# Performance work log

Hardware: AMD Instinct MI355X
Metric: run time of the kernel (lower is better)

The kernel has to match this reference:

```python
import jax, jax.numpy as jnp
import numpy as np

N = 50000      # nodes
E = 800000     # edges (before self-loops)
DIN = 146      # input feature dim
D = 128        # hidden/out dim
G = 64         # graphs in batch
L = 4          # number of GCNConv layers (len(hidden_dims[1:]) + 1)
NC = 10        # classes
EPS = 1e-5     # BatchNorm eps


def setup_inputs() -> dict:
    key = jax.random.key(0)
    ks = jax.random.split(key, 12)
    x = jax.random.normal(ks[0], (N, DIN), jnp.float32)
    edge_index = jax.random.randint(ks[1], (2, E), 0, N, dtype=jnp.int64)
    batch = jnp.sort(jax.random.randint(ks[2], (N,), 0, G, dtype=jnp.int64))

    def lin(k, shape, fan_in):
        return (jax.random.normal(k, shape, jnp.float32) / np.sqrt(fan_in)).astype(jnp.float32)

    W_emb = lin(ks[3], (DIN, D), DIN)
    b_emb = jnp.zeros((D,), jnp.float32)
    W_gcn = lin(ks[4], (L, D, D), D)
    b_gcn = jnp.zeros((L, D), jnp.float32)
    bn_gamma = jnp.ones((L, D), jnp.float32)
    bn_beta = jnp.zeros((L, D), jnp.float32)
    W_r1 = lin(ks[5], (D, D // 2), D)
    b_r1 = jnp.zeros((D // 2,), jnp.float32)
    W_r2 = lin(ks[6], (D // 2, D // 4), D // 2)
    b_r2 = jnp.zeros((D // 4,), jnp.float32)
    W_r3 = lin(ks[7], (D // 4, NC), D // 4)
    b_r3 = jnp.zeros((NC,), jnp.float32)
    return {"x": x, "edge_index": edge_index, "batch": batch,
            "W_emb": W_emb, "b_emb": b_emb, "W_gcn": W_gcn, "b_gcn": b_gcn,
            "bn_gamma": bn_gamma, "bn_beta": bn_beta,
            "W_r1": W_r1, "b_r1": b_r1, "W_r2": W_r2, "b_r2": b_r2,
            "W_r3": W_r3, "b_r3": b_r3}


def reference(x, edge_index, batch, W_emb, b_emb, W_gcn, b_gcn,
              bn_gamma, bn_beta, W_r1, b_r1, W_r2, b_r2, W_r3, b_r3):
    # gcn_norm with self-loops (fill_value=1, improved=False)
    loop = jnp.arange(N, dtype=edge_index.dtype)
    src = jnp.concatenate([edge_index[0], loop])
    dst = jnp.concatenate([edge_index[1], loop])
    deg = jax.ops.segment_sum(jnp.ones(src.shape, x.dtype), dst, num_segments=N)
    dinv = jax.lax.rsqrt(jnp.maximum(deg, jnp.asarray(1e-12, x.dtype)))  # deg >= 1 (self loops)
    norm = (dinv[src] * dinv[dst])[:, None]  # [E+N, 1]

    h = x @ W_emb + b_emb  # embedding_h
    for l in range(L):
        h_in = h
        m = h @ W_gcn[l]                                            # [N, D]
        h = jax.ops.segment_sum(m[src] * norm, dst, num_segments=N) + b_gcn[l]
        # BatchNorm1d (training-mode batch stats, biased var)
        mu = h.mean(axis=0)
        var = h.var(axis=0)
        h = (h - mu) * jax.lax.rsqrt(var + EPS) * bn_gamma[l] + bn_beta[l]
        h = jax.nn.relu(h)
        h = h_in + h  # residual (dims always match here)

    # global_mean_pool over batch ids
    sums = jax.ops.segment_sum(h, batch, num_segments=G)
    cnts = jax.ops.segment_sum(jnp.ones((N, 1), h.dtype), batch, num_segments=G)
    hg = sums / jnp.maximum(cnts, 1.0)

    # MLPReadout: two hidden layers halving dims, then classifier
    z = jax.nn.relu(hg @ W_r1 + b_r1)
    z = jax.nn.relu(z @ W_r2 + b_r2)
    return z @ W_r3 + b_r3  # [G, NC]
```

## Files before the change

### kernel.cpp

```cpp
#include <hip/hip_runtime.h>
#include <hip/hip_bf16.h>

#define NN 50000
#define EE 800000
#define DIN 146
#define DD 128
#define GG 64
#define LL 4
#define NC 10
#define BN_EPS 1e-5f

#define KP_EMB 160
#define AST_L  136
#define NCOPY 64
#define NPW 4
#define RST 129

#define NBKT 196
#define BHP  200
#define NBE  782

#define A_EDGE   NBE
#define A_INIT   (A_EDGE + 256)
#define A_REPACK (A_INIT + 31250)
#define A_BATCH  (A_REPACK + 196)
#define A_PARAMS (A_BATCH + 384)
#define A_WT     (A_PARAMS + 400)

#define B_GEMM 391
#define C_TOT  (B_GEMM + NBE)

typedef __attribute__((ext_vector_type(8))) short bf16x8;
typedef __attribute__((ext_vector_type(4))) float f32x4;

__device__ __forceinline__ float bf2f(__hip_bfloat16 v) { return __bfloat162float(v); }
__device__ __forceinline__ float loadf(const void* p, long i, int f32) {
    return f32 ? ((const float*)p)[i] : bf2f(((const __hip_bfloat16*)p)[i]);
}
__device__ __forceinline__ unsigned short f2bf_bits(float f) {
    __hip_bfloat16 h = __float2bfloat16(f);
    return *(unsigned short*)&h;
}
__device__ __forceinline__ float bfu2f(unsigned short u) {
    return __uint_as_float((unsigned)u << 16);
}
__device__ __forceinline__ void acc_add8(float* acc, uint4 v) {
    acc[0] += __uint_as_float(v.x << 16);
    acc[1] += __uint_as_float(v.x & 0xffff0000u);
    acc[2] += __uint_as_float(v.y << 16);
    acc[3] += __uint_as_float(v.y & 0xffff0000u);
    acc[4] += __uint_as_float(v.z << 16);
    acc[5] += __uint_as_float(v.z & 0xffff0000u);
    acc[6] += __uint_as_float(v.w << 16);
    acc[7] += __uint_as_float(v.w & 0xffff0000u);
}
__device__ __forceinline__ ushort4 pack4(f32x4 v) {
    ushort4 u;
    u.x = f2bf_bits(v[0]); u.y = f2bf_bits(v[1]);
    u.z = f2bf_bits(v[2]); u.w = f2bf_bits(v[3]);
    return u;
}
__device__ __forceinline__ ushort4 pack4s(f32x4 v, float s) {
    ushort4 u;
    u.x = f2bf_bits(s * v[0]); u.y = f2bf_bits(s * v[1]);
    u.z = f2bf_bits(s * v[2]); u.w = f2bf_bits(s * v[3]);
    return u;
}

__device__ __forceinline__ int blk_excl_scan(int v, int t, int* wsum, int* total_sh) {
    __syncthreads();
    int lane = t & 63, w = t >> 6;
    int x = v;
    #pragma unroll
    for (int s = 1; s < 64; s <<= 1) {
        int y = __shfl_up(x, s, 64);
        if (lane >= s) x += y;
    }
    if (lane == 63) wsum[w] = x;
    __syncthreads();
    if (t == 0) {
        int a = 0;
        #pragma unroll
        for (int k = 0; k < 4; ++k) { int tmp = wsum[k]; wsum[k] = a; a += tmp; }
        *total_sh = a;
    }
    __syncthreads();
    return x - v + wsum[w];
}

__global__ void detect_kernel(const void* ei, const void* batch, const void* Wemb,
                              int* __restrict__ flags) {
    __shared__ int s_edge_nz, s_batch_nz, s_f32_cnt;
    int t = threadIdx.x;
    if (t == 0) { s_edge_nz = 0; s_batch_nz = 0; s_f32_cnt = 0; }
    __syncthreads();
    {   const int* w = (const int*)ei;
        long j = ((long)t * ((2L * EE) / 64)) | 1;
        if (w[j] != 0) atomicAdd(&s_edge_nz, 1);
    }
    {   const int* w = (const int*)batch;
        long j = ((long)(NN / 2) + (long)t * ((NN / 2) / 64)) | 1;
        if (j < NN && w[j] != 0) atomicAdd(&s_batch_nz, 1);
    }
    {   const unsigned short* w = (const unsigned short*)Wemb;
        unsigned short v = w[2 * t];
        int ex = (v >> 7) & 0xFF;
        if (v != 0 && ex >= 128) atomicAdd(&s_f32_cnt, 1);
    }
    __syncthreads();
    if (t == 0) {
        flags[0] = (s_edge_nz == 0) ? 1 : 0;
        flags[1] = (s_batch_nz == 0) ? 1 : 0;
        flags[2] = (s_f32_cnt >= 8) ? 1 : 0;
    }
}

struct Param { const void* src; float* dst; int src_n; int dst_n; };
struct Params12 { Param p[12]; };
struct WtDesc { const void* src; long src_off; unsigned short* dst; int K; int Kpad; };
struct WtDescs5 { WtDesc p[5]; };

__global__ __launch_bounds__(256) void mega_conv_kernel(
    const void* __restrict__ x, const void* __restrict__ ei,
    const void* __restrict__ batch, const int* __restrict__ flags,
    unsigned short* __restrict__ xb, float* __restrict__ statmulti,
    float* __restrict__ hgsum, int* __restrict__ b32,
    unsigned* __restrict__ pk, unsigned char* __restrict__ bkt,
    int* __restrict__ bh, Params12 P, WtDescs5 W)
{
    int b = blockIdx.x;
    int t = threadIdx.x;
    if (b < A_EDGE) {
        __shared__ int hist[NBKT];
        if (t < NBKT) hist[t] = 0;
        __syncthreads();
        int e0 = (b * 256 + t) * 4;
        if (e0 < EE) {
            const int* w = (const int*)ei;
            int4 sv, dv;
            if (flags[0]) {
                int4 u0 = *(const int4*)(w + 2L * e0);
                int4 u1 = *(const int4*)(w + 2L * e0 + 4);
                int4 v0 = *(const int4*)(w + 2L * (EE + e0));
                int4 v1 = *(const int4*)(w + 2L * (EE + e0) + 4);
                sv = make_int4(u0.x, u0.z, u1.x, u1.z);
                dv = make_int4(v0.x, v0.z, v1.x, v1.z);
            } else {
                sv = *(const int4*)(w + e0);
                dv = *(const int4*)(w + EE + e0);
            }
            int ss[4] = {sv.x, sv.y, sv.z, sv.w};
            int dd2[4] = {dv.x, dv.y, dv.z, dv.w};
            unsigned pk4[4], bk4[4];
            #pragma unroll
            for (int k = 0; k < 4; ++k) {
                unsigned s = min((unsigned)ss[k], (unsigned)(NN - 1));
                unsigned d = min((unsigned)dd2[k], (unsigned)(NN - 1));
                pk4[k] = (s << 8) | (d & 255u);
                bk4[k] = d >> 8;
                atomicAdd(&hist[bk4[k]], 1);
            }
            *(uint4*)(pk + e0) = make_uint4(pk4[0], pk4[1], pk4[2], pk4[3]);
            *(uchar4*)(bkt + e0) = make_uchar4((unsigned char)bk4[0], (unsigned char)bk4[1],
                                               (unsigned char)bk4[2], (unsigned char)bk4[3]);
        }
        __syncthreads();
        if (t < NBKT) bh[b * BHP + t] = hist[t];
    } else if (b < A_INIT) {
        int i = (b - A_EDGE) * 256 + t;
        if (i < LL * NCOPY * 256) statmulti[i] = 0.0f;
        if (i < GG * DD) hgsum[i] = 0.0f;
    } else if (b < A_REPACK) {
        int f32 = flags[2];
        long idx = (long)(b - A_INIT) * 256 + t;
        int row = (int)(idx / KP_EMB);
        int k = (int)(idx - (long)row * KP_EMB);
        float v = (k < DIN) ? loadf(x, (long)row * DIN + k, f32) : 0.0f;
        xb[idx] = f2bf_bits(v);
    } else if (b < A_BATCH) {
        int i = (b - A_REPACK) * 256 + t;
        if (i < NN) b32[i] = flags[1] ? ((const int*)batch)[2L * i] : ((const int*)batch)[i];
    } else if (b < A_PARAMS) {
        int f32 = flags[2];
        int bb = b - A_BATCH;
        const Param& e = P.p[bb >> 5];
        int idx = (bb & 31) * 256 + t;
        if (idx < e.dst_n)
            e.dst[idx] = (idx < e.src_n) ? loadf(e.src, idx, f32) : 0.0f;
    } else {
        int f32 = flags[2];
        int bb = b - A_PARAMS;
        int y = bb / 80;
        const WtDesc& e = W.p[y];
        int idx = (bb - y * 80) * 256 + t;
        if (idx < 128 * e.Kpad) {
            int n = idx / e.Kpad, k = idx - n * e.Kpad;
            float v = (k < e.K) ? loadf(e.src, e.src_off + (long)k * DD + n, f32) : 0.0f;
            e.dst[idx] = f2bf_bits(v);
        }
    }
}

__global__ __launch_bounds__(256) void bscan_kernel(int* __restrict__ bh, int* __restrict__ tot) {
    __shared__ int wsum[4], total_sh;
    int b = blockIdx.x;
    int t = threadIdx.x;
    int carry = 0;
    #pragma unroll 1
    for (int c = 0; c < 4; ++c) {
        int i = c * 256 + t;
        int v = (i < NBE) ? bh[i * BHP + b] : 0;
        int excl = blk_excl_scan(v, t, wsum, &total_sh);
        if (i < NBE) bh[i * BHP + b] = excl + carry;
        carry += total_sh;
    }
    if (t == 0) tot[b] = carry;
}

__global__ void bscan2_kernel(const int* __restrict__ tot, int* __restrict__ base,
                              int* __restrict__ off_last) {
    __shared__ int wsum[4], total_sh;
    int t = threadIdx.x;
    int v = (t < NBKT) ? tot[t] : 0;
    int excl = blk_excl_scan(v, t, wsum, &total_sh);
    if (t < NBKT) base[t] = excl;
    if (t == 0) { base[NBKT] = total_sh; *off_last = total_sh; }
}


__global__ __launch_bounds__(256) void bucket_emb_kernel(
    const unsigned* __restrict__ pk, const unsigned char* __restrict__ bkt,
    const int* __restrict__ bh, const int* __restrict__ base,
    unsigned* __restrict__ bucketA,
    const unsigned short* __restrict__ Ab,
    const unsigned short* __restrict__ Wt,
    const float* __restrict__ bias,
    unsigned short* __restrict__ hb, int n)
{
    int t = threadIdx.x;
    if (blockIdx.x >= B_GEMM) {
        int bb = blockIdx.x - B_GEMM;
        __shared__ int cur[NBKT];
        if (t < NBKT) cur[t] = bh[bb * BHP + t] + base[t];
        __syncthreads();
        int e0 = (bb * 256 + t) * 4;
        if (e0 < EE) {
            uint4 p4 = *(const uint4*)(pk + e0);
            uchar4 b4 = *(const uchar4*)(bkt + e0);
            unsigned pks[4] = {p4.x, p4.y, p4.z, p4.w};
            unsigned bks[4] = {b4.x, b4.y, b4.z, b4.w};
            #pragma unroll
            for (int k = 0; k < 4; ++k) {
                int slot = atomicAdd(&cur[bks[k]], 1);
                bucketA[slot] = pks[k];
            }
        }
        return;
    }
    int r0 = blockIdx.x * 128;
    int lane = t & 63, w = t >> 6;
    int m = lane & 15, quad = lane >> 4;
    int rbase = r0 + w * 32;
    bf16x8 a[2][5];
    #pragma unroll
    for (int rt = 0; rt < 2; ++rt)
        #pragma unroll
        for (int c = 0; c < 5; ++c) {
            int rr = rbase + rt * 16 + m; if (rr > n - 1) rr = n - 1;
            a[rt][c] = *(const bf16x8*)(Ab + (long)rr * KP_EMB + c * 32 + quad * 8);
        }
    f32x4 acc[2][8];
    #pragma unroll
    for (int t8 = 0; t8 < 8; ++t8) {
        float4 bv = *(const float4*)&bias[t8 * 16 + quad * 4];
        f32x4 ai = {bv.x, bv.y, bv.z, bv.w};
        acc[0][t8] = ai; acc[1][t8] = ai;
    }
    #pragma unroll
    for (int t8 = 0; t8 < 8; ++t8) {
        #pragma unroll
        for (int c = 0; c < 5; ++c) {
            bf16x8 b = *(const bf16x8*)(Wt + (long)(t8 * 16 + m) * KP_EMB + c * 32 + quad * 8);
            acc[0][t8] = __builtin_amdgcn_mfma_f32_16x16x32_bf16(b, a[0][c], acc[0][t8], 0, 0, 0);
            acc[1][t8] = __builtin_amdgcn_mfma_f32_16x16x32_bf16(b, a[1][c], acc[1][t8], 0, 0, 0);
        }
    }
    #pragma unroll
    for (int rt = 0; rt < 2; ++rt) {
        int row = rbase + rt * 16 + m;
        if (row < n) {
            #pragma unroll
            for (int t8 = 0; t8 < 8; ++t8)
                *(ushort4*)(hb + (long)row * DD + t8 * 16 + quad * 4) = pack4(acc[rt][t8]);
        }
    }
}

__global__ __launch_bounds__(256) void csr_kernel(
    const unsigned* __restrict__ bucketA, const int* __restrict__ base,
    int* __restrict__ off, float* __restrict__ dinv, int* __restrict__ src_s)
{
    __shared__ int dg[256], cur[256], wsum[4], total_sh;
    int b = blockIdx.x, t = threadIdx.x;
    int eb0 = base[b], eb1 = base[b + 1];
    dg[t] = 0;
    __syncthreads();
    for (int e = eb0 + t; e < eb1; e += 256)
        atomicAdd(&dg[bucketA[e] & 255u], 1);
    __syncthreads();
    int v = dg[t];
    int excl = blk_excl_scan(v, t, wsum, &total_sh);
    int node = b * 256 + t;
    if (node < NN) {
        off[node] = eb0 + excl;
        dinv[node] = rsqrtf((float)(v + 1));
    }
    cur[t] = excl;
    __syncthreads();
    for (int e = eb0 + t; e < eb1; e += 256) {
        unsigned pv = bucketA[e];
        int r = atomicAdd(&cur[pv & 255u], 1);
        src_s[eb0 + r] = (int)(pv >> 8);
    }
}

__global__ __launch_bounds__(256) void gemm_plain_kernel(
    const unsigned short* __restrict__ Ab,
    const unsigned short* __restrict__ Wt,
    const float* __restrict__ dinv,
    unsigned short* __restrict__ Mb, int n)
{
    int t = threadIdx.x;
    int r0 = blockIdx.x * 128;
    int lane = t & 63, w = t >> 6;
    int m = lane & 15, quad = lane >> 4;
    int rbase = r0 + w * 32;
    bf16x8 a[2][4];
    #pragma unroll
    for (int rt = 0; rt < 2; ++rt)
        #pragma unroll
        for (int c = 0; c < 4; ++c) {
            int rr = rbase + rt * 16 + m; if (rr > n - 1) rr = n - 1;
            a[rt][c] = *(const bf16x8*)(Ab + (long)rr * DD + c * 32 + quad * 8);
        }
    float dvt[2];
    int rowt[2];
    #pragma unroll
    for (int rt = 0; rt < 2; ++rt) {
        int rr = rbase + rt * 16 + m;
        rowt[rt] = rr;
        if (rr > n - 1) rr = n - 1;
        dvt[rt] = dinv[rr];
    }
    f32x4 acc[2][8];
    #pragma unroll
    for (int t8 = 0; t8 < 8; ++t8) {
        f32x4 z = {0.f, 0.f, 0.f, 0.f};
        acc[0][t8] = z; acc[1][t8] = z;
    }
    #pragma unroll
    for (int t8 = 0; t8 < 8; ++t8) {
        #pragma unroll
        for (int c = 0; c < 4; ++c) {
            bf16x8 b = *(const bf16x8*)(Wt + (long)(t8 * 16 + m) * DD + c * 32 + quad * 8);
            acc[0][t8] = __builtin_amdgcn_mfma_f32_16x16x32_bf16(b, a[0][c], acc[0][t8], 0, 0, 0);
            acc[1][t8] = __builtin_amdgcn_mfma_f32_16x16x32_bf16(b, a[1][c], acc[1][t8], 0, 0, 0);
        }
    }
    #pragma unroll
    for (int rt = 0; rt < 2; ++rt) {
        if (rowt[rt] < n) {
            #pragma unroll
            for (int t8 = 0; t8 < 8; ++t8)
                *(ushort4*)(Mb + (long)rowt[rt] * DD + t8 * 16 + quad * 4) = pack4s(acc[rt][t8], dvt[rt]);
        }
    }
}

__global__ __launch_bounds__(256) void gemm_fused_kernel(
    const unsigned short* __restrict__ aggb, unsigned short* __restrict__ hb,
    const float* __restrict__ statmulti, const float* __restrict__ gamma,
    const float* __restrict__ beta, const float* __restrict__ dinv,
    const unsigned short* __restrict__ Wt, unsigned short* __restrict__ Mb, int n)
{
    __shared__ unsigned short As[128 * AST_L];
    __shared__ float bnsh[256];
    int t = threadIdx.x;
    int r0 = blockIdx.x * 128;
    {
        float s = 0.0f;
        #pragma unroll 8
        for (int k = 0; k < NCOPY; ++k) s += statmulti[k * 256 + t];
        bnsh[t] = s;
    }
    __syncthreads();
    {
        int c4 = (t & 31) * 4, rsub = t >> 5;
        float inv_n = 1.0f / (float)n;
        float4 sm = *(const float4*)&bnsh[c4];
        float4 sq = *(const float4*)&bnsh[128 + c4];
        float4 ga = *(const float4*)&gamma[c4];
        float4 be = *(const float4*)&beta[c4];
        float4 mu, rs;
        mu.x = sm.x * inv_n; mu.y = sm.y * inv_n; mu.z = sm.z * inv_n; mu.w = sm.w * inv_n;
        rs.x = rsqrtf(sq.x * inv_n - mu.x * mu.x + BN_EPS) * ga.x;
        rs.y = rsqrtf(sq.y * inv_n - mu.y * mu.y + BN_EPS) * ga.y;
        rs.z = rsqrtf(sq.z * inv_n - mu.z * mu.z + BN_EPS) * ga.z;
        rs.w = rsqrtf(sq.w * inv_n - mu.w * mu.w + BN_EPS) * ga.w;
        #pragma unroll 4
        for (int i = 0; i < 16; ++i) {
            int row = i * 8 + rsub;
            int r = r0 + row;
            unsigned short o0 = 0, o1 = 0, o2 = 0, o3 = 0;
            if (r < n) {
                long g = (long)r * DD + c4;
                ushort4 au = *(const ushort4*)&aggb[g];
                ushort4 hu = *(const ushort4*)&hb[g];
                float h0 = bfu2f(hu.x) + fmaxf((bfu2f(au.x) - mu.x) * rs.x + be.x, 0.0f);
                float h1 = bfu2f(hu.y) + fmaxf((bfu2f(au.y) - mu.y) * rs.y + be.y, 0.0f);
                float h2 = bfu2f(hu.z) + fmaxf((bfu2f(au.z) - mu.z) * rs.z + be.z, 0.0f);
                float h3 = bfu2f(hu.w) + fmaxf((bfu2f(au.w) - mu.w) * rs.w + be.w, 0.0f);
                o0 = f2bf_bits(h0); o1 = f2bf_bits(h1);
                o2 = f2bf_bits(h2); o3 = f2bf_bits(h3);
                ushort4 ho; ho.x = o0; ho.y = o1; ho.z = o2; ho.w = o3;
                *(ushort4*)&hb[g] = ho;
            }
            unsigned short* dst = &As[row * AST_L + c4];
            dst[0] = o0; dst[1] = o1; dst[2] = o2; dst[3] = o3;
        }
    }
    __syncthreads();
    int lane = t & 63, w = t >> 6;
    int m = lane & 15, quad = lane >> 4;
    int rl = w * 32;
    int rbase = r0 + rl;
    bf16x8 a[2][4];
    #pragma unroll
    for (int rt = 0; rt < 2; ++rt)
        #pragma unroll
        for (int c = 0; c < 4; ++c)
            a[rt][c] = *(const bf16x8*)(As + (rl + rt * 16 + m) * AST_L + c * 32 + quad * 8);
    float dvt[2];
    int rowt[2];
    #pragma unroll
    for (int rt = 0; rt < 2; ++rt) {
        int rr = rbase + rt * 16 + m;
        rowt[rt] = rr;
        if (rr > n - 1) rr = n - 1;
        dvt[rt] = dinv[rr];
    }
    f32x4 acc[2][8];
    #pragma unroll
    for (int t8 = 0; t8 < 8; ++t8) {
        f32x4 z = {0.f, 0.f, 0.f, 0.f};
        acc[0][t8] = z; acc[1][t8] = z;
    }
    #pragma unroll
    for (int t8 = 0; t8 < 8; ++t8) {
        #pragma unroll
        for (int c = 0; c < 4; ++c) {
            bf16x8 b = *(const bf16x8*)(Wt + (long)(t8 * 16 + m) * DD + c * 32 + quad * 8);
            acc[0][t8] = __builtin_amdgcn_mfma_f32_16x16x32_bf16(b, a[0][c], acc[0][t8], 0, 0, 0);
            acc[1][t8] = __builtin_amdgcn_mfma_f32_16x16x32_bf16(b, a[1][c], acc[1][t8], 0, 0, 0);
        }
    }
    #pragma unroll
    for (int rt = 0; rt < 2; ++rt) {
        if (rowt[rt] < n) {
            #pragma unroll
            for (int t8 = 0; t8 < 8; ++t8)
                *(ushort4*)(Mb + (long)rowt[rt] * DD + t8 * 16 + quad * 4) = pack4s(acc[rt][t8], dvt[rt]);
        }
    }
}

__global__ __launch_bounds__(256) void agg_kernel(
    const unsigned short* __restrict__ mb, const int* __restrict__ off,
    const int* __restrict__ src_s,
    const float* __restrict__ dinv, const float* __restrict__ bias,
    unsigned short* __restrict__ aggb, float* __restrict__ statacc)
{
    __shared__ float sred[4][4 * RST];
    __shared__ float2 ssum[4][64], ssq[4][64];
    int t = threadIdx.x;
    int wv = t >> 6, lane = t & 63;
    int grp = lane >> 4, sl = lane & 15;
    float* red = sred[wv];
    float2 bi = ((const float2*)bias)[lane];
    float2 sAcc = {0.0f, 0.0f}, qAcc = {0.0f, 0.0f};
    int i0 = (blockIdx.x * 4 + wv) * NPW;
    #pragma unroll 1
    for (int ni = 0; ni < NPW; ++ni) {
        int i = i0 + ni;
        if (i >= NN) break;
        float acc[8];
        #pragma unroll
        for (int k = 0; k < 8; ++k) acc[k] = 0.0f;
        if (grp == 0) {
            uint4 v = *(const uint4*)(mb + (long)i * DD + sl * 8);
            acc_add8(acc, v);
        }
        int e  = off[i];
        int e1 = off[i + 1];
        for (; e + 16 <= e1; e += 16) {
            int j0 = src_s[e + grp];
            int j1 = src_s[e + 4 + grp];
            int j2 = src_s[e + 8 + grp];
            int j3 = src_s[e + 12 + grp];
            uint4 v0 = *(const uint4*)(mb + (long)j0 * DD + sl * 8);
            uint4 v1 = *(const uint4*)(mb + (long)j1 * DD + sl * 8);
            uint4 v2 = *(const uint4*)(mb + (long)j2 * DD + sl * 8);
            uint4 v3 = *(const uint4*)(mb + (long)j3 * DD + sl * 8);
            acc_add8(acc, v0);
            acc_add8(acc, v1);
            acc_add8(acc, v2);
            acc_add8(acc, v3);
        }
        for (; e + 8 <= e1; e += 8) {
            int ja = src_s[e + grp];
            int jb = src_s[e + 4 + grp];
            uint4 va = *(const uint4*)(mb + (long)ja * DD + sl * 8);
            uint4 vb = *(const uint4*)(mb + (long)jb * DD + sl * 8);
            acc_add8(acc, va);
            acc_add8(acc, vb);
        }
        for (; e + 4 <= e1; e += 4) {
            int j = src_s[e + grp];
            uint4 v = *(const uint4*)(mb + (long)j * DD + sl * 8);
            acc_add8(acc, v);
        }
        if (e + grp < e1) {
            int j = src_s[e + grp];
            uint4 v = *(const uint4*)(mb + (long)j * DD + sl * 8);
            acc_add8(acc, v);
        }
        #pragma unroll
        for (int k = 0; k < 8; ++k) red[grp * RST + sl * 8 + k] = acc[k];
        asm volatile("" ::: "memory");
        float c0 = 0.0f, c1 = 0.0f;
        #pragma unroll
        for (int g = 0; g < 4; ++g) {
            c0 += red[g * RST + 2 * lane];
            c1 += red[g * RST + 2 * lane + 1];
        }
        asm volatile("" ::: "memory");
        float di = dinv[i];
        float o0 = di * c0 + bi.x;
        float o1 = di * c1 + bi.y;
        unsigned packed = ((unsigned)f2bf_bits(o1) << 16) | f2bf_bits(o0);
        ((unsigned*)aggb)[(long)i * 64 + lane] = packed;
        sAcc.x += o0; sAcc.y += o1;
        qAcc.x += o0 * o0; qAcc.y += o1 * o1;
    }
    ssum[wv][lane] = sAcc; ssq[wv][lane] = qAcc;
    __syncthreads();
    if (wv == 0) {
        float2 s0 = ssum[0][lane], s1 = ssum[1][lane], s2 = ssum[2][lane], s3 = ssum[3][lane];
        float2 q0 = ssq[0][lane], q1 = ssq[1][lane], q2 = ssq[2][lane], q3 = ssq[3][lane];
        float sx = s0.x + s1.x + s2.x + s3.x;
        float sy = s0.y + s1.y + s2.y + s3.y;
        float qx = q0.x + q1.x + q2.x + q3.x;
        float qy = q0.y + q1.y + q2.y + q3.y;
        float* copy = statacc + (blockIdx.x & (NCOPY - 1)) * 256;
        atomicAdd(&copy[2 * lane], sx);
        atomicAdd(&copy[2 * lane + 1], sy);
        atomicAdd(&copy[128 + 2 * lane], qx);
        atomicAdd(&copy[128 + 2 * lane + 1], qy);
    }
}

__global__ void pool1_kernel(const unsigned short* __restrict__ hb,
                             const unsigned short* __restrict__ aggb,
                             const float* __restrict__ statmulti,
                             const float* __restrict__ gamma, const float* __restrict__ beta,
                             const int* __restrict__ b32, float* __restrict__ hgsum, int n) {
    __shared__ float bnsh[256];
    int t = threadIdx.x;
    {
        float s = 0.0f;
        #pragma unroll 8
        for (int k = 0; k < NCOPY; ++k) s += statmulti[k * 256 + t];
        bnsh[t] = s;
    }
    __syncthreads();
    int c4 = (t & 31) * 4, rsub = t >> 5;
    float inv_n = 1.0f / (float)n;
    float4 sm = *(const float4*)&bnsh[c4];
    float4 sq = *(const float4*)&bnsh[128 + c4];
    float4 ga = *(const float4*)&gamma[c4];
    float4 be = *(const float4*)&beta[c4];
    float4 mu, rs;
    mu.x = sm.x * inv_n; mu.y = sm.y * inv_n; mu.z = sm.z * inv_n; mu.w = sm.w * inv_n;
    rs.x = rsqrtf(sq.x * inv_n - mu.x * mu.x + BN_EPS) * ga.x;
    rs.y = rsqrtf(sq.y * inv_n - mu.y * mu.y + BN_EPS) * ga.y;
    rs.z = rsqrtf(sq.z * inv_n - mu.z * mu.z + BN_EPS) * ga.z;
    rs.w = rsqrtf(sq.w * inv_n - mu.w * mu.w + BN_EPS) * ga.w;
    int rows_pb = (n + gridDim.x - 1) / gridDim.x;
    int r0 = blockIdx.x * rows_pb;
    int r1 = min(n, r0 + rows_pb);
    float4 acc = {0, 0, 0, 0};
    int gcur = -1;
    for (int r = r0 + rsub; r < r1; r += 8) {
        int g = b32[r];
        if (g != gcur) {
            if (gcur >= 0) {
                atomicAdd(&hgsum[gcur * DD + c4 + 0], acc.x);
                atomicAdd(&hgsum[gcur * DD + c4 + 1], acc.y);
                atomicAdd(&hgsum[gcur * DD + c4 + 2], acc.z);
                atomicAdd(&hgsum[gcur * DD + c4 + 3], acc.w);
            }
            acc.x = acc.y = acc.z = acc.w = 0.0f;
            gcur = ((unsigned)g < (unsigned)GG) ? g : -1;
        }
        if (gcur >= 0) {
            long ix = (long)r * DD + c4;
            ushort4 au = *(const ushort4*)&aggb[ix];
            ushort4 hu = *(const ushort4*)&hb[ix];
            acc.x += bfu2f(hu.x) + fmaxf((bfu2f(au.x) - mu.x) * rs.x + be.x, 0.0f);
            acc.y += bfu2f(hu.y) + fmaxf((bfu2f(au.y) - mu.y) * rs.y + be.y, 0.0f);
            acc.z += bfu2f(hu.z) + fmaxf((bfu2f(au.z) - mu.z) * rs.z + be.z, 0.0f);
            acc.w += bfu2f(hu.w) + fmaxf((bfu2f(au.w) - mu.w) * rs.w + be.w, 0.0f);
        }
    }
    if (gcur >= 0) {
        atomicAdd(&hgsum[gcur * DD + c4 + 0], acc.x);
        atomicAdd(&hgsum[gcur * DD + c4 + 1], acc.y);
        atomicAdd(&hgsum[gcur * DD + c4 + 2], acc.z);
        atomicAdd(&hgsum[gcur * DD + c4 + 3], acc.w);
    }
}

__device__ int lower_bound_i(const int* __restrict__ a, int n, int v) {
    int lo = 0, hi = n;
    while (lo < hi) {
        int mid = (lo + hi) >> 1;
        if (a[mid] < v) lo = mid + 1; else hi = mid;
    }
    return lo;
}

__global__ void readout_kernel(const float* __restrict__ hgsum, const int* __restrict__ b32,
                               const float* __restrict__ W1, const float* __restrict__ b1,
                               const float* __restrict__ W2, const float* __restrict__ b2,
                               const float* __restrict__ W3, const float* __restrict__ b3,
                               const int* __restrict__ flags, void* __restrict__ out, int n) {
    int f32 = flags[2];
    int g = blockIdx.x;
    int t = threadIdx.x;
    __shared__ float hgs[DD];
    __shared__ float z1[DD / 2];
    __shared__ float z2[DD / 4];
    int lo = lower_bound_i(b32, n, g);
    int hi = lower_bound_i(b32, n, g + 1);
    float invc = 1.0f / fmaxf((float)(hi - lo), 1.0f);
    hgs[t] = hgsum[g * DD + t] * invc;
    __syncthreads();
    if (t < DD / 2) {
        float acc = b1[t];
        #pragma unroll 8
        for (int k = 0; k < DD; ++k) acc = fmaf(hgs[k], W1[k * (DD / 2) + t], acc);
        z1[t] = fmaxf(acc, 0.0f);
    }
    __syncthreads();
    if (t < DD / 4) {
        float acc = b2[t];
        #pragma unroll 8
        for (int k = 0; k < DD / 2; ++k) acc = fmaf(z1[k], W2[k * (DD / 4) + t], acc);
        z2[t] = fmaxf(acc, 0.0f);
    }
    __syncthreads();
    if (t < NC) {
        float acc = b3[t];
        #pragma unroll 8
        for (int k = 0; k < DD / 4; ++k) acc = fmaf(z2[k], W3[k * NC + t], acc);
        if (f32) ((float*)out)[g * NC + t] = acc;
        else     ((__hip_bfloat16*)out)[g * NC + t] = __float2bfloat16(acc);
    }
}

extern "C" void kernel_launch(void* const* d_in, const int* in_sizes, int n_in,
                              void* d_out, int out_size, void* d_ws, size_t ws_size,
                              hipStream_t stream) {
    const void* x      = d_in[0];
    const void* ei     = d_in[1];
    const void* batch  = d_in[2];
    const void* W_emb  = d_in[3];
    const void* b_emb  = d_in[4];
    const void* W_gcn  = d_in[5];
    const void* b_gcn  = d_in[6];
    const void* bn_g   = d_in[7];
    const void* bn_b   = d_in[8];
    const void* W_r1   = d_in[9];
    const void* b_r1   = d_in[10];
    const void* W_r2   = d_in[11];
    const void* b_r2   = d_in[12];
    const void* W_r3   = d_in[13];
    const void* b_r3   = d_in[14];

    char* p = (char*)d_ws;
    auto alloc = [&](size_t bytes) -> void* {
        void* r = (void*)p;
        p += (bytes + 255) & ~(size_t)255;
        return r;
    };
    int*   flags  = (int*)alloc(64 * 4);
    float* statmulti = (float*)alloc((size_t)LL * NCOPY * 256 * 4);
    float* hgsum  = (float*)alloc((size_t)GG * DD * 4);
    int*   off    = (int*)alloc((size_t)(NN + 1) * 4);
    float* dinv   = (float*)alloc((size_t)NN * 4);
    int*   b32    = (int*)alloc((size_t)NN * 4);
    int*   src_s  = (int*)alloc((size_t)EE * 4);
    unsigned* pk  = (unsigned*)alloc((size_t)EE * 4);
    unsigned char* bkt = (unsigned char*)alloc((size_t)EE);
    int*   bh     = (int*)alloc((size_t)NBE * BHP * 4);
    int*   tot    = (int*)alloc(256 * 4);
    int*   base   = (int*)alloc(256 * 4);
    unsigned* bucketA = (unsigned*)alloc((size_t)EE * 4);
    unsigned short* hb = (unsigned short*)alloc((size_t)NN * DD * 2);
    unsigned short* mb = (unsigned short*)alloc((size_t)NN * DD * 2);
    unsigned short* aggb = (unsigned short*)alloc((size_t)NN * DD * 2);
    unsigned short* xb = (unsigned short*)alloc((size_t)NN * KP_EMB * 2);
    unsigned short* wt_emb = (unsigned short*)alloc((size_t)DD * KP_EMB * 2);
    unsigned short* wt_gcn = (unsigned short*)alloc((size_t)LL * DD * DD * 2);
    float* b_emb32 = (float*)alloc(DD * 4);
    float* b_gcn32 = (float*)alloc((size_t)LL * DD * 4);
    float* bng32   = (float*)alloc((size_t)LL * DD * 4);
    float* bnb32   = (float*)alloc((size_t)LL * DD * 4);
    float* wr1     = (float*)alloc((size_t)DD * (DD / 2) * 4);
    float* br1     = (float*)alloc((DD / 2) * 4);
    float* wr2     = (float*)alloc((size_t)(DD / 2) * (DD / 4) * 4);
    float* br2     = (float*)alloc((DD / 4) * 4);
    float* wr3     = (float*)alloc((size_t)(DD / 4) * NC * 4);
    float* br3     = (float*)alloc(NC * 4);

    detect_kernel<<<1, 64, 0, stream>>>(ei, batch, W_emb, flags);

    Params12 P;
    P.p[0]  = { b_emb, b_emb32, DD, DD };
    P.p[1]  = { b_gcn, b_gcn32, LL * DD, LL * DD };
    P.p[2]  = { bn_g,  bng32,   LL * DD, LL * DD };
    P.p[3]  = { bn_b,  bnb32,   LL * DD, LL * DD };
    P.p[4]  = { W_r1,  wr1,     DD * (DD / 2), DD * (DD / 2) };
    P.p[5]  = { b_r1,  br1,     DD / 2, DD / 2 };
    P.p[6]  = { W_r2,  wr2,     (DD / 2) * (DD / 4), (DD / 2) * (DD / 4) };
    P.p[7]  = { b_r2,  br2,     DD / 4, DD / 4 };
    P.p[8]  = { W_r3,  wr3,     (DD / 4) * NC, (DD / 4) * NC };
    P.p[9]  = { b_r3,  br3,     NC, NC };
    P.p[10] = { b_r3,  br3,     0, 0 };
    P.p[11] = { b_r3,  br3,     0, 0 };

    WtDescs5 W;
    W.p[0] = { W_emb, 0,            wt_emb,                DIN, KP_EMB };
    W.p[1] = { W_gcn, 0L * DD * DD, wt_gcn + 0L * DD * DD, DD,  DD };
    W.p[2] = { W_gcn, 1L * DD * DD, wt_gcn + 1L * DD * DD, DD,  DD };
    W.p[3] = { W_gcn, 2L * DD * DD, wt_gcn + 2L * DD * DD, DD,  DD };
    W.p[4] = { W_gcn, 3L * DD * DD, wt_gcn + 3L * DD * DD, DD,  DD };

    mega_conv_kernel<<<A_WT, 256, 0, stream>>>(x, ei, batch, flags, xb, statmulti,
                                               hgsum, b32, pk, bkt, bh, P, W);

    bscan_kernel<<<NBKT, 256, 0, stream>>>(bh, tot);
    bscan2_kernel<<<1, 256, 0, stream>>>(tot, base, off + NN);

    bucket_emb_kernel<<<C_TOT, 256, 0, stream>>>(pk, bkt, bh, base, bucketA,
                                                 xb, wt_emb, b_emb32, hb, NN);

    csr_kernel<<<NBKT, 256, 0, stream>>>(bucketA, base, off, dinv, src_s);

    gemm_plain_kernel<<<(NN + 127) / 128, 256, 0, stream>>>(hb, wt_gcn, dinv, mb, NN);

    int ngemm = (NN + 127) / 128;
    int nagg = (NN + 4 * NPW - 1) / (4 * NPW);
    for (int l = 0; l < LL; ++l) {
        if (l > 0) {
            gemm_fused_kernel<<<ngemm, 256, 0, stream>>>(
                aggb, hb, statmulti + (size_t)(l - 1) * NCOPY * 256,
                bng32 + (l - 1) * DD, bnb32 + (l - 1) * DD,
                dinv, wt_gcn + (size_t)l * DD * DD, mb, NN);
        }
        agg_kernel<<<nagg, 256, 0, stream>>>(mb, off, src_s, dinv,
                                             b_gcn32 + l * DD, aggb,
                                             statmulti + (size_t)l * NCOPY * 256);
    }

    pool1_kernel<<<512, 256, 0, stream>>>(hb, aggb, statmulti + (size_t)(LL - 1) * NCOPY * 256,
                                          bng32 + (LL - 1) * DD, bnb32 + (LL - 1) * DD,
                                          b32, hgsum, NN);
    readout_kernel<<<GG, DD, 0, stream>>>(hgsum, b32, wr1, br1, wr2, br2, wr3, br3,
                                          flags, d_out, NN);
}
```

Measured before the change: 413.3 us.

## Aggregate full rows per wave lane-wise and vectorize input repacking

```diff
diff --git a/kernel.cpp b/kernel.cpp
--- a/kernel.cpp
+++ b/kernel.cpp
@@ -14,7 +14,6 @@
 #define AST_L  136
 #define NCOPY 64
 #define NPW 4
-#define RST 129
 
 #define NBKT 196
 #define BHP  200
@@ -22,7 +21,7 @@
 
 #define A_EDGE   NBE
 #define A_INIT   (A_EDGE + 256)
-#define A_REPACK (A_INIT + 31250)
+#define A_REPACK (A_INIT + 3907)
 #define A_BATCH  (A_REPACK + 196)
 #define A_PARAMS (A_BATCH + 384)
 #define A_WT     (A_PARAMS + 400)
@@ -44,16 +43,8 @@
 __device__ __forceinline__ float bfu2f(unsigned short u) {
     return __uint_as_float((unsigned)u << 16);
 }
-__device__ __forceinline__ void acc_add8(float* acc, uint4 v) {
-    acc[0] += __uint_as_float(v.x << 16);
-    acc[1] += __uint_as_float(v.x & 0xffff0000u);
-    acc[2] += __uint_as_float(v.y << 16);
-    acc[3] += __uint_as_float(v.y & 0xffff0000u);
-    acc[4] += __uint_as_float(v.z << 16);
-    acc[5] += __uint_as_float(v.z & 0xffff0000u);
-    acc[6] += __uint_as_float(v.w << 16);
-    acc[7] += __uint_as_float(v.w & 0xffff0000u);
-}
+__device__ __forceinline__ float lo16(unsigned v) { return __uint_as_float(v << 16); }
+__device__ __forceinline__ float hi16(unsigned v) { return __uint_as_float(v & 0xffff0000u); }
 __device__ __forceinline__ ushort4 pack4(f32x4 v) {
     ushort4 u;
     u.x = f2bf_bits(v[0]); u.y = f2bf_bits(v[1]);
@@ -172,11 +163,43 @@
         if (i < GG * DD) hgsum[i] = 0.0f;
     } else if (b < A_REPACK) {
         int f32 = flags[2];
-        long idx = (long)(b - A_INIT) * 256 + t;
-        int row = (int)(idx / KP_EMB);
-        int k = (int)(idx - (long)row * KP_EMB);
-        float v = (k < DIN) ? loadf(x, (long)row * DIN + k, f32) : 0.0f;
-        xb[idx] = f2bf_bits(v);
+        long idx8 = (long)(b - A_INIT) * 256 + t;
+        if (idx8 < (long)NN * 20) {
+            int row = (int)(idx8 / 20);
+            int c8 = (int)(idx8 - (long)row * 20) * 8;
+            float v[8];
+            if (c8 + 8 <= DIN) {
+                if (f32) {
+                    const float* xp = (const float*)x + (long)row * DIN + c8;
+                    #pragma unroll
+                    for (int k2 = 0; k2 < 4; ++k2) {
+                        float2 f = *(const float2*)(xp + 2 * k2);
+                        v[2 * k2] = f.x; v[2 * k2 + 1] = f.y;
+                    }
+                } else {
+                    const unsigned* xp = (const unsigned*)((const unsigned short*)x +
+                                                           (long)row * DIN + c8);
+                    #pragma unroll
+                    for (int k2 = 0; k2 < 4; ++k2) {
+                        unsigned u = xp[k2];
+                        v[2 * k2] = bfu2f((unsigned short)u);
+                        v[2 * k2 + 1] = bfu2f((unsigned short)(u >> 16));
+                    }
+                }
+            } else {
+                #pragma unroll
+                for (int k = 0; k < 8; ++k) {
+                    int col = c8 + k;
+                    v[k] = (col < DIN) ? loadf(x, (long)row * DIN + col, f32) : 0.0f;
+                }
+            }
+            unsigned o[4];
+            #pragma unroll
+            for (int k2 = 0; k2 < 4; ++k2)
+                o[k2] = (unsigned)f2bf_bits(v[2 * k2]) |
+                        ((unsigned)f2bf_bits(v[2 * k2 + 1]) << 16);
+            *(uint4*)(xb + (long)row * KP_EMB + c8) = make_uint4(o[0], o[1], o[2], o[3]);
+        }
     } else if (b < A_BATCH) {
         int i = (b - A_REPACK) * 256 + t;
         if (i < NN) b32[i] = flags[1] ? ((const int*)batch)[2L * i] : ((const int*)batch)[i];
@@ -475,17 +498,14 @@
 }
 
 __global__ __launch_bounds__(256) void agg_kernel(
-    const unsigned short* __restrict__ mb, const int* __restrict__ off,
+    const unsigned* __restrict__ mb32, const int* __restrict__ off,
     const int* __restrict__ src_s,
     const float* __restrict__ dinv, const float* __restrict__ bias,
-    unsigned short* __restrict__ aggb, float* __restrict__ statacc)
+    unsigned* __restrict__ aggb32, float* __restrict__ statacc)
 {
-    __shared__ float sred[4][4 * RST];
     __shared__ float2 ssum[4][64], ssq[4][64];
     int t = threadIdx.x;
     int wv = t >> 6, lane = t & 63;
-    int grp = lane >> 4, sl = lane & 15;
-    float* red = sred[wv];
     float2 bi = ((const float2*)bias)[lane];
     float2 sAcc = {0.0f, 0.0f}, qAcc = {0.0f, 0.0f};
     int i0 = (blockIdx.x * 4 + wv) * NPW;
@@ -493,62 +513,49 @@
     for (int ni = 0; ni < NPW; ++ni) {
         int i = i0 + ni;
         if (i >= NN) break;
-        float acc[8];
-        #pragma unroll
-        for (int k = 0; k < 8; ++k) acc[k] = 0.0f;
-        if (grp == 0) {
-            uint4 v = *(const uint4*)(mb + (long)i * DD + sl * 8);
-            acc_add8(acc, v);
-        }
-        int e  = off[i];
-        int e1 = off[i + 1];
-        for (; e + 16 <= e1; e += 16) {
-            int j0 = src_s[e + grp];
-            int j1 = src_s[e + 4 + grp];
-            int j2 = src_s[e + 8 + grp];
-            int j3 = src_s[e + 12 + grp];
-            uint4 v0 = *(const uint4*)(mb + (long)j0 * DD + sl * 8);
-            uint4 v1 = *(const uint4*)(mb + (long)j1 * DD + sl * 8);
-            uint4 v2 = *(const uint4*)(mb + (long)j2 * DD + sl * 8);
-            uint4 v3 = *(const uint4*)(mb + (long)j3 * DD + sl * 8);
-            acc_add8(acc, v0);
-            acc_add8(acc, v1);
-            acc_add8(acc, v2);
-            acc_add8(acc, v3);
-        }
+        int e = off[i], e1 = off[i + 1];
+        unsigned vs = mb32[(long)i * 64 + lane];
+        float a0 = lo16(vs), a1 = hi16(vs);
         for (; e + 8 <= e1; e += 8) {
-            int ja = src_s[e + grp];
-            int jb = src_s[e + 4 + grp];
-            uint4 va = *(const uint4*)(mb + (long)ja * DD + sl * 8);
-            uint4 vb = *(const uint4*)(mb + (long)jb * DD + sl * 8);
-            acc_add8(acc, va);
-            acc_add8(acc, vb);
+            int j0 = src_s[e + 0], j1 = src_s[e + 1], j2 = src_s[e + 2], j3 = src_s[e + 3];
+            int j4 = src_s[e + 4], j5 = src_s[e + 5], j6 = src_s[e + 6], j7 = src_s[e + 7];
+            unsigned v0 = mb32[(long)j0 * 64 + lane];
+            unsigned v1 = mb32[(long)j1 * 64 + lane];
+            unsigned v2 = mb32[(long)j2 * 64 + lane];
+            unsigned v3 = mb32[(long)j3 * 64 + lane];
+            unsigned v4 = mb32[(long)j4 * 64 + lane];
+            unsigned v5 = mb32[(long)j5 * 64 + lane];
+            unsigned v6 = mb32[(long)j6 * 64 + lane];
+            unsigned v7 = mb32[(long)j7 * 64 + lane];
+            a0 += lo16(v0); a1 += hi16(v0);
+            a0 += lo16(v1); a1 += hi16(v1);
+            a0 += lo16(v2); a1 += hi16(v2);
+            a0 += lo16(v3); a1 += hi16(v3);
+            a0 += lo16(v4); a1 += hi16(v4);
+            a0 += lo16(v5); a1 += hi16(v5);
+            a0 += lo16(v6); a1 += hi16(v6);
+            a0 += lo16(v7); a1 += hi16(v7);
         }
         for (; e + 4 <= e1; e += 4) {
-            int j = src_s[e + grp];
-            uint4 v = *(const uint4*)(mb + (long)j * DD + sl * 8);
-            acc_add8(acc, v);
-        }
-        if (e + grp < e1) {
-            int j = src_s[e + grp];
-            uint4 v = *(const uint4*)(mb + (long)j * DD + sl * 8);
-            acc_add8(acc, v);
-        }
-        #pragma unroll
-        for (int k = 0; k < 8; ++k) red[grp * RST + sl * 8 + k] = acc[k];
-        asm volatile("" ::: "memory");
-        float c0 = 0.0f, c1 = 0.0f;
-        #pragma unroll
-        for (int g = 0; g < 4; ++g) {
-            c0 += red[g * RST + 2 * lane];
-            c1 += red[g * RST + 2 * lane + 1];
-        }
-        asm volatile("" ::: "memory");
+            int j0 = src_s[e + 0], j1 = src_s[e + 1], j2 = src_s[e + 2], j3 = src_s[e + 3];
+            unsigned v0 = mb32[(long)j0 * 64 + lane];
+            unsigned v1 = mb32[(long)j1 * 64 + lane];
+            unsigned v2 = mb32[(long)j2 * 64 + lane];
+            unsigned v3 = mb32[(long)j3 * 64 + lane];
+            a0 += lo16(v0); a1 += hi16(v0);
+            a0 += lo16(v1); a1 += hi16(v1);
+            a0 += lo16(v2); a1 += hi16(v2);
+            a0 += lo16(v3); a1 += hi16(v3);
+        }
+        for (; e < e1; ++e) {
+            int j = src_s[e];
+            unsigned v = mb32[(long)j * 64 + lane];
+            a0 += lo16(v); a1 += hi16(v);
+        }
         float di = dinv[i];
-        float o0 = di * c0 + bi.x;
-        float o1 = di * c1 + bi.y;
-        unsigned packed = ((unsigned)f2bf_bits(o1) << 16) | f2bf_bits(o0);
-        ((unsigned*)aggb)[(long)i * 64 + lane] = packed;
+        float o0 = fmaf(di, a0, bi.x);
+        float o1 = fmaf(di, a1, bi.y);
+        aggb32[(long)i * 64 + lane] = ((unsigned)f2bf_bits(o1) << 16) | f2bf_bits(o0);
         sAcc.x += o0; sAcc.y += o1;
         qAcc.x += o0 * o0; qAcc.y += o1 * o1;
     }
@@ -778,8 +785,8 @@
                 bng32 + (l - 1) * DD, bnb32 + (l - 1) * DD,
                 dinv, wt_gcn + (size_t)l * DD * DD, mb, NN);
         }
-        agg_kernel<<<nagg, 256, 0, stream>>>(mb, off, src_s, dinv,
-                                             b_gcn32 + l * DD, aggb,
+        agg_kernel<<<nagg, 256, 0, stream>>>((const unsigned*)mb, off, src_s, dinv,
+                                             b_gcn32 + l * DD, (unsigned*)aggb,
                                              statmulti + (size_t)l * NCOPY * 256);
     }
 
```

Result: slower. 422.7 us (+2.3%).
